# Kernel optimization log

Measured on AMD Instinct MI355X. Metric: run time of the kernel, lower is better.

## Reference

```python
import jax, jax.numpy as jnp
import numpy as np

N_NODES = 100000
N_EDGES = 1600000
IN_C, HID_C, OUT_C = 128, 64, 32


def setup_inputs() -> dict:
    key = jax.random.key(0)
    k0, k1, k2, k3 = jax.random.split(key, 4)
    x = jax.random.normal(k0, (N_NODES, IN_C), dtype=jnp.float32)
    edge_index = jax.random.randint(k1, (2, N_EDGES), 0, N_NODES, dtype=jnp.int32)
    # Glorot-ish init for GCNConv weights, zero bias (PyG default bias init is zeros)
    W1 = jax.random.normal(k2, (IN_C, HID_C), dtype=jnp.float32) * (1.0 / np.sqrt(IN_C))
    b1 = jnp.zeros((HID_C,), dtype=jnp.float32)
    W2 = jax.random.normal(k3, (HID_C, OUT_C), dtype=jnp.float32) * (1.0 / np.sqrt(HID_C))
    b2 = jnp.zeros((OUT_C,), dtype=jnp.float32)
    return {"x": x, "edge_index": edge_index, "W1": W1, "b1": b1, "W2": W2, "b2": b2}


def reference(x, edge_index, W1, b1, W2, b2):
    n = x.shape[0]
    # GCNConv default: add self-loops, then symmetric normalization D^-1/2 A D^-1/2
    loop = jnp.arange(n, dtype=edge_index.dtype)
    src = jnp.concatenate([edge_index[0], loop])  # message sources (j)
    dst = jnp.concatenate([edge_index[1], loop])  # aggregation targets (i)
    deg = jax.ops.segment_sum(jnp.ones(src.shape, x.dtype), dst, num_segments=n)
    inv_sqrt = jnp.where(deg > 0, jax.lax.rsqrt(deg), 0.0)
    norm = inv_sqrt[src] * inv_sqrt[dst]  # [E+N]

    def gcn_conv(h, W, b):
        h = h @ W  # transform first (smaller feature dim for aggregation)
        msgs = h[src] * norm[:, None]  # gather + scale, [E+N, d]
        agg = jax.ops.segment_sum(msgs, dst, num_segments=n)  # scatter-add
        return agg + b

    h = jax.nn.relu(gcn_conv(x, W1, b1))
    return gcn_conv(h, W2, b2)
```

## Files before the change

### kernel.cpp

```cpp
#include <hip/hip_runtime.h>

#define N_NODES 100000
#define N_EDGES 1600000
#define NCOARSE 391
#define CB_NODES 256
#define CSTRIPE 8
#define CCAP    704
#define CSTRIDE 5632
#define BCHUNKS 256
#define BCHUNK  6250
#define NSTRIPS 6250

typedef short short8 __attribute__((ext_vector_type(8)));
typedef float f32x4 __attribute__((ext_vector_type(4)));
union Frag { uint4 q; short8 s; };

__device__ inline unsigned short f2bf(float f) {
    unsigned u = __float_as_uint(f);
    unsigned r = u + 0x7fffu + ((u >> 16) & 1u);
    return (unsigned short)(r >> 16);
}
__device__ inline unsigned pk2(float lo, float hi) {
    return (unsigned)f2bf(lo) | ((unsigned)f2bf(hi) << 16);
}
__device__ inline float bflo(unsigned u) { return __uint_as_float(u << 16); }
__device__ inline float bfhi(unsigned u) { return __uint_as_float(u & 0xffff0000u); }

__global__ __launch_bounds__(256) void k_prep(const float* __restrict__ W1, const float* __restrict__ W2,
                                              unsigned* __restrict__ W1f, unsigned* __restrict__ W2f,
                                              int* __restrict__ cbcnt) {
    int f = blockIdx.x;
    int t = threadIdx.x;
    if (f >= 20) {
        int i = (f - 20) * 256 + t;
        if (i < NCOARSE * CSTRIPE) cbcnt[i] = 0;
        return;
    }
    int lane = t >> 2, w = t & 3;
    if (f < 16) {
        int ks = f >> 2, ct = f & 3;
        int col = ct * 16 + (lane & 15);
        int k = ks * 32 + (lane >> 4) * 8 + 2 * w;
        W1f[(f * 64 + lane) * 4 + w] = pk2(W1[k * 64 + col], W1[(k + 1) * 64 + col]);
    } else {
        int f2 = f - 16;
        int ks = f2 >> 1, ct = f2 & 1;
        int col = ct * 16 + (lane & 15);
        int k = ks * 32 + (lane >> 4) * 8 + 2 * w;
        W2f[(f2 * 64 + lane) * 4 + w] = pk2(W2[k * 32 + col], W2[(k + 1) * 32 + col]);
    }
}

__global__ __launch_bounds__(512) void k_bin(const int* __restrict__ ei, unsigned* __restrict__ pairs,
                                             int* __restrict__ cbcnt) {
    __shared__ int hist[NCOARSE];
    __shared__ int base[NCOARSE];
    int t = threadIdx.x;
    int chunk = blockIdx.x;
    int s = chunk & (CSTRIPE - 1);
    int e0 = chunk * BCHUNK;
    int e1 = e0 + BCHUNK;
    for (int i = t; i < NCOARSE; i += 512) hist[i] = 0;
    __syncthreads();
#pragma unroll 4
    for (int e = e0 + t; e < e1; e += 512) {
        atomicAdd(&hist[ei[N_EDGES + e] >> 8], 1);
    }
    __syncthreads();
    for (int i = t; i < NCOARSE; i += 512) {
        int h = hist[i];
        if (h > 0) base[i] = atomicAdd(&cbcnt[i * CSTRIPE + s], h);
        hist[i] = 0;
    }
    __syncthreads();
#pragma unroll 2
    for (int e = e0 + t; e < e1; e += 512) {
        int src = ei[e];
        int dst = ei[N_EDGES + e];
        int b = dst >> 8;
        int r = atomicAdd(&hist[b], 1);
        int pos = base[b] + r;
        if (pos < CCAP)
            pairs[(size_t)(b * CSTRIPE + s) * CCAP + pos] = ((unsigned)src << 8) | (unsigned)(dst & 255);
    }
}

__global__ __launch_bounds__(256) void k_csr(const unsigned* __restrict__ pairs, const int* __restrict__ cbcnt,
                                             int* __restrict__ cols, int2* __restrict__ rpc,
                                             float* __restrict__ invs) {
    __shared__ unsigned ep[CSTRIDE];
    __shared__ unsigned srt[CSTRIDE];
    __shared__ int scnt[CSTRIPE];
    __shared__ int sbase[CSTRIPE + 1];
    __shared__ int cnt[CB_NODES];
    __shared__ int cur[CB_NODES];
    __shared__ int wsum[4];
    int t = threadIdx.x;
    int b = blockIdx.x;
    if (t < CSTRIPE) {
        int c = cbcnt[b * CSTRIPE + t];
        scnt[t] = (c < CCAP) ? c : CCAP;
    }
    cnt[t] = 0;
    __syncthreads();
    if (t == 0) {
        int acc = 0;
#pragma unroll
        for (int s = 0; s < CSTRIPE; ++s) { sbase[s] = acc; acc += scnt[s]; }
        sbase[CSTRIPE] = acc;
    }
    __syncthreads();
    int n = sbase[CSTRIPE];
#pragma unroll
    for (int s = 0; s < CSTRIPE; ++s) {
        int cs = scnt[s];
        const unsigned* sp = pairs + (size_t)(b * CSTRIPE + s) * CCAP;
        const uint4* sp4 = (const uint4*)sp;
        int base = sbase[s];
        int cs4 = cs >> 2;
        for (int i = t; i < cs4; i += 256) {
            uint4 v = sp4[i];
            int o = base + i * 4;
            ep[o] = v.x; ep[o + 1] = v.y; ep[o + 2] = v.z; ep[o + 3] = v.w;
        }
        for (int i = cs4 * 4 + t; i < cs; i += 256) ep[base + i] = sp[i];
    }
    __syncthreads();
    for (int i = t; i < n; i += 256) atomicAdd(&cnt[ep[i] & 255u], 1);
    __syncthreads();
    {
        int c = cnt[t];
        int v = c;
#pragma unroll
        for (int off = 1; off < 64; off <<= 1) {
            int u = __shfl_up(v, off, 64);
            if ((t & 63) >= off) v += u;
        }
        if ((t & 63) == 63) wsum[t >> 6] = v;
        __syncthreads();
        int woff = 0;
        for (int w = 0; w < (t >> 6); ++w) woff += wsum[w];
        int excl = woff + v - c;
        cur[t] = excl;
        int node = b * CB_NODES + t;
        if (node < N_NODES) {
            rpc[node] = make_int2(b * CSTRIDE + excl, c);
            invs[node] = rsqrtf((float)(c + 1));
        }
    }
    __syncthreads();
    for (int i = t; i < n; i += 256) {
        unsigned p = ep[i];
        int f = p & 255u;
        int pos = atomicAdd(&cur[f], 1);
        srt[pos] = p >> 8;
    }
    __syncthreads();
    int* outp = cols + (size_t)b * CSTRIDE;
    uint4* outp4 = (uint4*)outp;
    int n4 = n >> 2;
    for (int i = t; i < n4; i += 256) {
        int o = i * 4;
        outp4[i] = make_uint4(srt[o], srt[o + 1], srt[o + 2], srt[o + 3]);
    }
    for (int i = n4 * 4 + t; i < n; i += 256) outp[i] = (int)srt[i];
}

__global__ __launch_bounds__(256) void k_gemm1(const float* __restrict__ X, const uint4* __restrict__ W1f,
                                               const float* __restrict__ invs, unsigned short* __restrict__ out) {
    __shared__ unsigned short lt[4][16][72];
    int t = threadIdx.x;
    int w = t >> 6, l = t & 63;
    int strip = blockIdx.x * 4 + w;
    if (strip >= NSTRIPS) return;
    const float* xrow = X + (size_t)(strip * 16 + (l & 15)) * 128;
    f32x4 acc[4];
#pragma unroll
    for (int ct = 0; ct < 4; ++ct) acc[ct] = (f32x4){0.f, 0.f, 0.f, 0.f};
#pragma unroll
    for (int ks = 0; ks < 4; ++ks) {
        int kk = ks * 32 + (l >> 4) * 8;
        float4 xa = *(const float4*)(xrow + kk);
        float4 xb = *(const float4*)(xrow + kk + 4);
        Frag fa;
        fa.q = make_uint4(pk2(xa.x, xa.y), pk2(xa.z, xa.w), pk2(xb.x, xb.y), pk2(xb.z, xb.w));
#pragma unroll
        for (int ct = 0; ct < 4; ++ct) {
            Frag fb; fb.q = W1f[(ks * 4 + ct) * 64 + l];
            acc[ct] = __builtin_amdgcn_mfma_f32_16x16x32_bf16(fa.s, fb.s, acc[ct], 0, 0, 0);
        }
    }
    int rbase = strip * 16 + (l >> 4) * 4;
    float iv0 = invs[rbase], iv1 = invs[rbase + 1], iv2 = invs[rbase + 2], iv3 = invs[rbase + 3];
#pragma unroll
    for (int ct = 0; ct < 4; ++ct) {
        int cc = ct * 16 + (l & 15);
        int rr = (l >> 4) * 4;
        lt[w][rr + 0][cc] = f2bf(acc[ct][0] * iv0);
        lt[w][rr + 1][cc] = f2bf(acc[ct][1] * iv1);
        lt[w][rr + 2][cc] = f2bf(acc[ct][2] * iv2);
        lt[w][rr + 3][cc] = f2bf(acc[ct][3] * iv3);
    }
    uint4* og = (uint4*)(out + (size_t)strip * 16 * 64);
#pragma unroll
    for (int it = 0; it < 2; ++it) {
        int idx = it * 64 + l;
        int row = idx >> 3, seg = idx & 7;
        og[idx] = *(const uint4*)&lt[w][row][seg * 8];
    }
}

__global__ __launch_bounds__(256) void k_l1(const unsigned short* __restrict__ hs, const int2* __restrict__ rpc,
                                            const int* __restrict__ col, const float* __restrict__ invs,
                                            const float* __restrict__ b1, const uint4* __restrict__ W2f,
                                            unsigned short* __restrict__ out) {
    __shared__ unsigned short hsh[32][72];
    __shared__ float ivsh[32];
    __shared__ uint4 w2sh[256];
    int t = threadIdx.x;
    w2sh[t] = W2f[t];
    int l = t & 7;
    int g = t >> 3;
    int node = blockIdx.x * 32 + g;
    int2 rc = rpc[node];
    int ps = rc.x, pe = rc.x + rc.y;
    const uint4* hv = (const uint4*)hs;
    float a0 = 0.f, a1 = 0.f, a2 = 0.f, a3 = 0.f, a4 = 0.f, a5 = 0.f, a6 = 0.f, a7 = 0.f;
    int p = ps;
    for (; p + 4 <= pe; p += 4) {
        int j0 = col[p], j1 = col[p + 1], j2 = col[p + 2], j3 = col[p + 3];
        uint4 u0 = hv[(size_t)j0 * 8 + l];
        uint4 u1 = hv[(size_t)j1 * 8 + l];
        uint4 u2 = hv[(size_t)j2 * 8 + l];
        uint4 u3 = hv[(size_t)j3 * 8 + l];
        a0 += bflo(u0.x); a1 += bfhi(u0.x); a2 += bflo(u0.y); a3 += bfhi(u0.y);
        a4 += bflo(u0.z); a5 += bfhi(u0.z); a6 += bflo(u0.w); a7 += bfhi(u0.w);
        a0 += bflo(u1.x); a1 += bfhi(u1.x); a2 += bflo(u1.y); a3 += bfhi(u1.y);
        a4 += bflo(u1.z); a5 += bfhi(u1.z); a6 += bflo(u1.w); a7 += bfhi(u1.w);
        a0 += bflo(u2.x); a1 += bfhi(u2.x); a2 += bflo(u2.y); a3 += bfhi(u2.y);
        a4 += bflo(u2.z); a5 += bfhi(u2.z); a6 += bflo(u2.w); a7 += bfhi(u2.w);
        a0 += bflo(u3.x); a1 += bfhi(u3.x); a2 += bflo(u3.y); a3 += bfhi(u3.y);
        a4 += bflo(u3.z); a5 += bfhi(u3.z); a6 += bflo(u3.w); a7 += bfhi(u3.w);
    }
    for (; p < pe; ++p) {
        uint4 u = hv[(size_t)col[p] * 8 + l];
        a0 += bflo(u.x); a1 += bfhi(u.x); a2 += bflo(u.y); a3 += bfhi(u.y);
        a4 += bflo(u.z); a5 += bfhi(u.z); a6 += bflo(u.w); a7 += bfhi(u.w);
    }
    uint4 us = hv[(size_t)node * 8 + l];
    a0 += bflo(us.x); a1 += bfhi(us.x); a2 += bflo(us.y); a3 += bfhi(us.y);
    a4 += bflo(us.z); a5 += bfhi(us.z); a6 += bflo(us.w); a7 += bfhi(us.w);
    float iv = invs[node];
    float4 bb0 = *(const float4*)&b1[l * 8];
    float4 bb1 = *(const float4*)&b1[l * 8 + 4];
    float h0 = fmaxf(a0 * iv + bb0.x, 0.f), h1 = fmaxf(a1 * iv + bb0.y, 0.f);
    float h2 = fmaxf(a2 * iv + bb0.z, 0.f), h3 = fmaxf(a3 * iv + bb0.w, 0.f);
    float h4 = fmaxf(a4 * iv + bb1.x, 0.f), h5 = fmaxf(a5 * iv + bb1.y, 0.f);
    float h6 = fmaxf(a6 * iv + bb1.z, 0.f), h7 = fmaxf(a7 * iv + bb1.w, 0.f);
    uint4 hw;
    hw.x = pk2(h0, h1); hw.y = pk2(h2, h3); hw.z = pk2(h4, h5); hw.w = pk2(h6, h7);
    *(uint4*)&hsh[g][l * 8] = hw;
    if (l == 0) ivsh[g] = iv;
    __syncthreads();
    int wv = t >> 6, lane = t & 63;
    int rt = wv & 1, ct = wv >> 1;
    f32x4 acc = (f32x4){0.f, 0.f, 0.f, 0.f};
#pragma unroll
    for (int ks = 0; ks < 2; ++ks) {
        Frag fa; fa.q = *(const uint4*)&hsh[rt * 16 + (lane & 15)][ks * 32 + (lane >> 4) * 8];
        Frag fb; fb.q = w2sh[(ks * 2 + ct) * 64 + lane];
        acc = __builtin_amdgcn_mfma_f32_16x16x32_bf16(fa.s, fb.s, acc, 0, 0, 0);
    }
    int rl = rt * 16 + (lane >> 4) * 4;
    size_t nodeo = (size_t)(blockIdx.x * 32 + rl);
    int cc = ct * 16 + (lane & 15);
    out[(nodeo + 0) * 32 + cc] = f2bf(acc[0] * ivsh[rl + 0]);
    out[(nodeo + 1) * 32 + cc] = f2bf(acc[1] * ivsh[rl + 1]);
    out[(nodeo + 2) * 32 + cc] = f2bf(acc[2] * ivsh[rl + 2]);
    out[(nodeo + 3) * 32 + cc] = f2bf(acc[3] * ivsh[rl + 3]);
}

__global__ __launch_bounds__(256) void k_spmm2(const unsigned short* __restrict__ hs, const int2* __restrict__ rpc,
                                               const int* __restrict__ col, const float* __restrict__ invs,
                                               const float* __restrict__ b, float* __restrict__ out) {
    int t = threadIdx.x;
    int l = t & 3;
    int node = blockIdx.x * 64 + (t >> 2);
    if (node >= N_NODES) return;
    int2 rc = rpc[node];
    int ps = rc.x, pe = rc.x + rc.y;
    const uint4* hv = (const uint4*)hs;
    float a0 = 0.f, a1 = 0.f, a2 = 0.f, a3 = 0.f, a4 = 0.f, a5 = 0.f, a6 = 0.f, a7 = 0.f;
    int p = ps;
    for (; p + 4 <= pe; p += 4) {
        int j0 = col[p], j1 = col[p + 1], j2 = col[p + 2], j3 = col[p + 3];
        uint4 u0 = hv[(size_t)j0 * 4 + l];
        uint4 u1 = hv[(size_t)j1 * 4 + l];
        uint4 u2 = hv[(size_t)j2 * 4 + l];
        uint4 u3 = hv[(size_t)j3 * 4 + l];
        a0 += bflo(u0.x); a1 += bfhi(u0.x); a2 += bflo(u0.y); a3 += bfhi(u0.y);
        a4 += bflo(u0.z); a5 += bfhi(u0.z); a6 += bflo(u0.w); a7 += bfhi(u0.w);
        a0 += bflo(u1.x); a1 += bfhi(u1.x); a2 += bflo(u1.y); a3 += bfhi(u1.y);
        a4 += bflo(u1.z); a5 += bfhi(u1.z); a6 += bflo(u1.w); a7 += bfhi(u1.w);
        a0 += bflo(u2.x); a1 += bfhi(u2.x); a2 += bflo(u2.y); a3 += bfhi(u2.y);
        a4 += bflo(u2.z); a5 += bfhi(u2.z); a6 += bflo(u2.w); a7 += bfhi(u2.w);
        a0 += bflo(u3.x); a1 += bfhi(u3.x); a2 += bflo(u3.y); a3 += bfhi(u3.y);
        a4 += bflo(u3.z); a5 += bfhi(u3.z); a6 += bflo(u3.w); a7 += bfhi(u3.w);
    }
    for (; p < pe; ++p) {
        uint4 u = hv[(size_t)col[p] * 4 + l];
        a0 += bflo(u.x); a1 += bfhi(u.x); a2 += bflo(u.y); a3 += bfhi(u.y);
        a4 += bflo(u.z); a5 += bfhi(u.z); a6 += bflo(u.w); a7 += bfhi(u.w);
    }
    uint4 us = hv[(size_t)node * 4 + l];
    a0 += bflo(us.x); a1 += bfhi(us.x); a2 += bflo(us.y); a3 += bfhi(us.y);
    a4 += bflo(us.z); a5 += bfhi(us.z); a6 += bflo(us.w); a7 += bfhi(us.w);
    float iv = invs[node];
    float4 bb0 = *(const float4*)&b[l * 8];
    float4 bb1 = *(const float4*)&b[l * 8 + 4];
    float4 oA = make_float4(a0 * iv + bb0.x, a1 * iv + bb0.y, a2 * iv + bb0.z, a3 * iv + bb0.w);
    float4 oB = make_float4(a4 * iv + bb1.x, a5 * iv + bb1.y, a6 * iv + bb1.z, a7 * iv + bb1.w);
    *(float4*)&out[(size_t)node * 32 + l * 8] = oA;
    *(float4*)&out[(size_t)node * 32 + l * 8 + 4] = oB;
}

extern "C" void kernel_launch(void* const* d_in, const int* in_sizes, int n_in,
                              void* d_out, int out_size, void* d_ws, size_t ws_size,
                              hipStream_t stream) {
    const float* x  = (const float*)d_in[0];
    const int*   ei = (const int*)d_in[1];
    const float* W1 = (const float*)d_in[2];
    const float* b1 = (const float*)d_in[3];
    const float* W2 = (const float*)d_in[4];
    const float* b2 = (const float*)d_in[5];
    float* out = (float*)d_out;

    char* ws = (char*)d_ws;
    size_t off = 0;
    auto alloc = [&](size_t bytes) -> void* {
        void* p = ws + off;
        off = (off + bytes + 255) & ~(size_t)255;
        return p;
    };
    int*            cbcnt = (int*)alloc((size_t)NCOARSE * CSTRIPE * 4);
    float*          invs  = (float*)alloc((size_t)N_NODES * 4);
    unsigned*       pairs = (unsigned*)alloc((size_t)NCOARSE * CSTRIPE * CCAP * 4);
    int*            cols  = (int*)alloc((size_t)NCOARSE * CSTRIDE * 4);
    int2*           rpc   = (int2*)alloc((size_t)N_NODES * 8);
    unsigned short* hs1   = (unsigned short*)alloc((size_t)N_NODES * 64 * 2);
    unsigned short* hs2   = (unsigned short*)alloc((size_t)N_NODES * 32 * 2);
    unsigned*       W1f   = (unsigned*)alloc(16 * 64 * 16);
    unsigned*       W2f   = (unsigned*)alloc(4 * 64 * 16);

    k_prep<<<20 + (NCOARSE * CSTRIPE + 255) / 256, 256, 0, stream>>>(W1, W2, W1f, W2f, cbcnt);
    k_bin<<<BCHUNKS, 512, 0, stream>>>(ei, pairs, cbcnt);
    k_csr<<<NCOARSE, 256, 0, stream>>>(pairs, cbcnt, cols, rpc, invs);
    k_gemm1<<<(NSTRIPS + 3) / 4, 256, 0, stream>>>(x, (const uint4*)W1f, invs, hs1);
    k_l1<<<N_NODES / 32, 256, 0, stream>>>(hs1, rpc, cols, invs, b1, (const uint4*)W2f, hs2);
    k_spmm2<<<(N_NODES + 63) / 64, 256, 0, stream>>>(hs2, rpc, cols, invs, b2, out);
}
```

Measured before the change: 108.0 us.

## Degree-sort nodes within each coarse bucket for balanced SpMM warps

In the CSR build, nodes within each 256-node bucket are counting-sorted by in-degree, and a slot-to-node map is written. The aggregation kernels then iterate over slots so that neighbouring groups in a wavefront have similar degrees, which reduces divergence and load imbalance. Outputs are scattered back through the node map, and padded slots past N_NODES are masked. Separately, the binning kernel now uses twice as many, smaller edge chunks. The cost is an extra indirection load and non-contiguous output writes.

```diff
diff --git a/kernel.cpp b/kernel.cpp
--- a/kernel.cpp
+++ b/kernel.cpp
@@ -4,11 +4,12 @@
 #define N_EDGES 1600000
 #define NCOARSE 391
 #define CB_NODES 256
+#define NSLOTS  (NCOARSE * CB_NODES)
 #define CSTRIPE 8
 #define CCAP    704
 #define CSTRIDE 5632
-#define BCHUNKS 256
-#define BCHUNK  6250
+#define BCHUNKS 512
+#define BCHUNK  3125
 #define NSTRIPS 6250
 
 typedef short short8 __attribute__((ext_vector_type(8)));
@@ -87,14 +88,19 @@
 
 __global__ __launch_bounds__(256) void k_csr(const unsigned* __restrict__ pairs, const int* __restrict__ cbcnt,
                                              int* __restrict__ cols, int2* __restrict__ rpc,
-                                             float* __restrict__ invs) {
+                                             int* __restrict__ nodeof, float* __restrict__ invs) {
     __shared__ unsigned ep[CSTRIDE];
     __shared__ unsigned srt[CSTRIDE];
     __shared__ int scnt[CSTRIPE];
     __shared__ int sbase[CSTRIPE + 1];
     __shared__ int cnt[CB_NODES];
     __shared__ int cur[CB_NODES];
-    __shared__ int wsum[4];
+    __shared__ int dh[64];
+    __shared__ int dcur[64];
+    __shared__ int sortcnt[CB_NODES];
+    __shared__ int rankof[CB_NODES];
+    __shared__ int sstart[CB_NODES];
+    __shared__ int wsum2[4];
     int t = threadIdx.x;
     int b = blockIdx.x;
     if (t < CSTRIPE) {
@@ -102,6 +108,7 @@
         scnt[t] = (c < CCAP) ? c : CCAP;
     }
     cnt[t] = 0;
+    if (t < 64) dh[t] = 0;
     __syncthreads();
     if (t == 0) {
         int acc = 0;
@@ -128,25 +135,49 @@
     __syncthreads();
     for (int i = t; i < n; i += 256) atomicAdd(&cnt[ep[i] & 255u], 1);
     __syncthreads();
-    {
-        int c = cnt[t];
+    int d = cnt[t];
+    int dc = (d < 63) ? d : 63;
+    atomicAdd(&dh[dc], 1);
+    __syncthreads();
+    if (t < 64) {
+        int c = dh[t];
         int v = c;
 #pragma unroll
         for (int off = 1; off < 64; off <<= 1) {
             int u = __shfl_up(v, off, 64);
-            if ((t & 63) >= off) v += u;
+            if (t >= off) v += u;
         }
-        if ((t & 63) == 63) wsum[t >> 6] = v;
+        dcur[t] = v - c;
+    }
+    __syncthreads();
+    int rank = atomicAdd(&dcur[dc], 1);
+    rankof[t] = rank;
+    sortcnt[rank] = d;
+    __syncthreads();
+    {
+        int c2 = sortcnt[t];
+        int v2 = c2;
+#pragma unroll
+        for (int off = 1; off < 64; off <<= 1) {
+            int u = __shfl_up(v2, off, 64);
+            if ((t & 63) >= off) v2 += u;
+        }
+        if ((t & 63) == 63) wsum2[t >> 6] = v2;
         __syncthreads();
         int woff = 0;
-        for (int w = 0; w < (t >> 6); ++w) woff += wsum[w];
-        int excl = woff + v - c;
-        cur[t] = excl;
+        for (int w = 0; w < (t >> 6); ++w) woff += wsum2[w];
+        sstart[t] = woff + v2 - c2;
+    }
+    __syncthreads();
+    {
+        int p = rankof[t];
+        int st = sstart[p];
+        cur[t] = st;
         int node = b * CB_NODES + t;
-        if (node < N_NODES) {
-            rpc[node] = make_int2(b * CSTRIDE + excl, c);
-            invs[node] = rsqrtf((float)(c + 1));
-        }
+        int slot = b * CB_NODES + p;
+        rpc[slot] = make_int2(b * CSTRIDE + st, d);
+        nodeof[slot] = node;
+        if (node < N_NODES) invs[node] = rsqrtf((float)(d + 1));
     }
     __syncthreads();
     for (int i = t; i < n; i += 256) {
@@ -211,18 +242,21 @@
 }
 
 __global__ __launch_bounds__(256) void k_l1(const unsigned short* __restrict__ hs, const int2* __restrict__ rpc,
-                                            const int* __restrict__ col, const float* __restrict__ invs,
+                                            const int* __restrict__ col, const int* __restrict__ nodeof,
+                                            const float* __restrict__ invs,
                                             const float* __restrict__ b1, const uint4* __restrict__ W2f,
                                             unsigned short* __restrict__ out) {
     __shared__ unsigned short hsh[32][72];
     __shared__ float ivsh[32];
+    __shared__ int ndsh[32];
     __shared__ uint4 w2sh[256];
     int t = threadIdx.x;
     w2sh[t] = W2f[t];
     int l = t & 7;
     int g = t >> 3;
-    int node = blockIdx.x * 32 + g;
-    int2 rc = rpc[node];
+    int slot = blockIdx.x * 32 + g;
+    int2 rc = rpc[slot];
+    int node = nodeof[slot];
     int ps = rc.x, pe = rc.x + rc.y;
     const uint4* hv = (const uint4*)hs;
     float a0 = 0.f, a1 = 0.f, a2 = 0.f, a3 = 0.f, a4 = 0.f, a5 = 0.f, a6 = 0.f, a7 = 0.f;
@@ -250,7 +284,7 @@
     uint4 us = hv[(size_t)node * 8 + l];
     a0 += bflo(us.x); a1 += bfhi(us.x); a2 += bflo(us.y); a3 += bfhi(us.y);
     a4 += bflo(us.z); a5 += bfhi(us.z); a6 += bflo(us.w); a7 += bfhi(us.w);
-    float iv = invs[node];
+    float iv = (node < N_NODES) ? invs[node] : 0.f;
     float4 bb0 = *(const float4*)&b1[l * 8];
     float4 bb1 = *(const float4*)&b1[l * 8 + 4];
     float h0 = fmaxf(a0 * iv + bb0.x, 0.f), h1 = fmaxf(a1 * iv + bb0.y, 0.f);
@@ -260,7 +294,7 @@
     uint4 hw;
     hw.x = pk2(h0, h1); hw.y = pk2(h2, h3); hw.z = pk2(h4, h5); hw.w = pk2(h6, h7);
     *(uint4*)&hsh[g][l * 8] = hw;
-    if (l == 0) ivsh[g] = iv;
+    if (l == 0) { ivsh[g] = iv; ndsh[g] = node; }
     __syncthreads();
     int wv = t >> 6, lane = t & 63;
     int rt = wv & 1, ct = wv >> 1;
@@ -272,22 +306,23 @@
         acc = __builtin_amdgcn_mfma_f32_16x16x32_bf16(fa.s, fb.s, acc, 0, 0, 0);
     }
     int rl = rt * 16 + (lane >> 4) * 4;
-    size_t nodeo = (size_t)(blockIdx.x * 32 + rl);
     int cc = ct * 16 + (lane & 15);
-    out[(nodeo + 0) * 32 + cc] = f2bf(acc[0] * ivsh[rl + 0]);
-    out[(nodeo + 1) * 32 + cc] = f2bf(acc[1] * ivsh[rl + 1]);
-    out[(nodeo + 2) * 32 + cc] = f2bf(acc[2] * ivsh[rl + 2]);
-    out[(nodeo + 3) * 32 + cc] = f2bf(acc[3] * ivsh[rl + 3]);
+#pragma unroll
+    for (int i = 0; i < 4; ++i) {
+        int nd = ndsh[rl + i];
+        if (nd < N_NODES) out[(size_t)nd * 32 + cc] = f2bf(acc[i] * ivsh[rl + i]);
+    }
 }
 
 __global__ __launch_bounds__(256) void k_spmm2(const unsigned short* __restrict__ hs, const int2* __restrict__ rpc,
-                                               const int* __restrict__ col, const float* __restrict__ invs,
+                                               const int* __restrict__ col, const int* __restrict__ nodeof,
+                                               const float* __restrict__ invs,
                                                const float* __restrict__ b, float* __restrict__ out) {
     int t = threadIdx.x;
     int l = t & 3;
-    int node = blockIdx.x * 64 + (t >> 2);
-    if (node >= N_NODES) return;
-    int2 rc = rpc[node];
+    int slot = blockIdx.x * 64 + (t >> 2);
+    int2 rc = rpc[slot];
+    int node = nodeof[slot];
     int ps = rc.x, pe = rc.x + rc.y;
     const uint4* hv = (const uint4*)hs;
     float a0 = 0.f, a1 = 0.f, a2 = 0.f, a3 = 0.f, a4 = 0.f, a5 = 0.f, a6 = 0.f, a7 = 0.f;
@@ -315,6 +350,7 @@
     uint4 us = hv[(size_t)node * 4 + l];
     a0 += bflo(us.x); a1 += bfhi(us.x); a2 += bflo(us.y); a3 += bfhi(us.y);
     a4 += bflo(us.z); a5 += bfhi(us.z); a6 += bflo(us.w); a7 += bfhi(us.w);
+    if (node >= N_NODES) return;
     float iv = invs[node];
     float4 bb0 = *(const float4*)&b[l * 8];
     float4 bb1 = *(const float4*)&b[l * 8 + 4];
@@ -342,20 +378,21 @@
         off = (off + bytes + 255) & ~(size_t)255;
         return p;
     };
-    int*            cbcnt = (int*)alloc((size_t)NCOARSE * CSTRIPE * 4);
-    float*          invs  = (float*)alloc((size_t)N_NODES * 4);
-    unsigned*       pairs = (unsigned*)alloc((size_t)NCOARSE * CSTRIPE * CCAP * 4);
-    int*            cols  = (int*)alloc((size_t)NCOARSE * CSTRIDE * 4);
-    int2*           rpc   = (int2*)alloc((size_t)N_NODES * 8);
-    unsigned short* hs1   = (unsigned short*)alloc((size_t)N_NODES * 64 * 2);
-    unsigned short* hs2   = (unsigned short*)alloc((size_t)N_NODES * 32 * 2);
-    unsigned*       W1f   = (unsigned*)alloc(16 * 64 * 16);
-    unsigned*       W2f   = (unsigned*)alloc(4 * 64 * 16);
+    int*            cbcnt  = (int*)alloc((size_t)NCOARSE * CSTRIPE * 4);
+    float*          invs   = (float*)alloc((size_t)N_NODES * 4);
+    unsigned*       pairs  = (unsigned*)alloc((size_t)NCOARSE * CSTRIPE * CCAP * 4);
+    int*            cols   = (int*)alloc((size_t)NCOARSE * CSTRIDE * 4);
+    int2*           rpc    = (int2*)alloc((size_t)NSLOTS * 8);
+    int*            nodeof = (int*)alloc((size_t)NSLOTS * 4);
+    unsigned short* hs1    = (unsigned short*)alloc((size_t)N_NODES * 64 * 2);
+    unsigned short* hs2    = (unsigned short*)alloc((size_t)N_NODES * 32 * 2);
+    unsigned*       W1f    = (unsigned*)alloc(16 * 64 * 16);
+    unsigned*       W2f    = (unsigned*)alloc(4 * 64 * 16);
 
     k_prep<<<20 + (NCOARSE * CSTRIPE + 255) / 256, 256, 0, stream>>>(W1, W2, W1f, W2f, cbcnt);
     k_bin<<<BCHUNKS, 512, 0, stream>>>(ei, pairs, cbcnt);
-    k_csr<<<NCOARSE, 256, 0, stream>>>(pairs, cbcnt, cols, rpc, invs);
+    k_csr<<<NCOARSE, 256, 0, stream>>>(pairs, cbcnt, cols, rpc, nodeof, invs);
     k_gemm1<<<(NSTRIPS + 3) / 4, 256, 0, stream>>>(x, (const uint4*)W1f, invs, hs1);
-    k_l1<<<N_NODES / 32, 256, 0, stream>>>(hs1, rpc, cols, invs, b1, (const uint4*)W2f, hs2);
-    k_spmm2<<<(N_NODES + 63) / 64, 256, 0, stream>>>(hs2, rpc, cols, invs, b2, out);
-}
+    k_l1<<<NSLOTS / 32, 256, 0, stream>>>(hs1, rpc, cols, nodeof, invs, b1, (const uint4*)W2f, hs2);
+    k_spmm2<<<NSLOTS / 64, 256, 0, stream>>>(hs2, rpc, cols, nodeof, invs, b2, out);
+}
```

Result: slower. 121.8 us (+12.8%).
